# Kernel tuning notes

Hardware: AMD Instinct MI355X
Metric: run time of the kernel (lower is better)

Reference implementation:

```python
import jax, jax.numpy as jnp
import numpy as np

B, LQ, LK, SIZE, H = 8, 1024, 1024, 512, 8


def setup_inputs() -> dict:
    key = jax.random.key(0)
    ks = jax.random.split(key, 12)
    scale = 1.0 / np.sqrt(SIZE)
    x = jax.random.normal(ks[0], (B, LQ, SIZE), dtype=jnp.float32)
    states = jax.random.normal(ks[1], (B, LK, SIZE), dtype=jnp.float32)
    mask = jax.random.randint(ks[2], (B, LQ, LK), 0, 2, dtype=jnp.int32)
    # Per-head full-size projections, stacked over heads: [H, size, size]
    Wq = jax.random.normal(ks[3], (H, SIZE, SIZE), dtype=jnp.float32) * scale
    bq = jnp.zeros((H, SIZE), dtype=jnp.float32)
    Wk = jax.random.normal(ks[4], (H, SIZE, SIZE), dtype=jnp.float32) * scale
    bk = jnp.zeros((H, SIZE), dtype=jnp.float32)
    Wv = jax.random.normal(ks[5], (H, SIZE, SIZE), dtype=jnp.float32) * scale
    bv = jnp.zeros((H, SIZE), dtype=jnp.float32)
    # Output projection: Linear(size*H, size); torch weight shape [size, size*H]
    Wp = jax.random.normal(ks[6], (SIZE, SIZE * H), dtype=jnp.float32) * (1.0 / np.sqrt(SIZE * H))
    bp = jnp.zeros((SIZE,), dtype=jnp.float32)
    return {"x": x, "states": states, "mask": mask,
            "Wq": Wq, "bq": bq, "Wk": Wk, "bk": bk, "Wv": Wv, "bv": bv,
            "Wp": Wp, "bp": bp}


def reference(x, states, mask, Wq, bq, Wk, bk, Wv, bv, Wp, bp):
    # torch Linear: y = x @ W.T + b ; W is [out,in] so contract over last axis 'e'
    q = jnp.einsum('bqe,hde->bhqd', x, Wq) + bq[:, None, :]       # [B,H,Lq,D]
    k = jnp.einsum('bke,hde->bhkd', states, Wk) + bk[:, None, :]  # [B,H,Lk,D]
    v = jnp.einsum('bke,hde->bhkd', states, Wv) + bv[:, None, :]  # [B,H,Lk,D]
    scores = jnp.einsum('bhqd,bhkd->bhqk', q, k) / jnp.sqrt(jnp.float32(SIZE))
    scores = jnp.where(mask[:, None, :, :] == 0, jnp.float32(-jnp.inf), scores)
    attn = jax.nn.softmax(scores, axis=-1)                        # softmax over Lk
    ctx = jnp.einsum('bhqk,bhkd->bhqd', attn, v)                  # [B,H,Lq,D]
    # concat heads in order -> [B, Lq, H*D]
    ctx = ctx.transpose(0, 2, 1, 3).reshape(B, LQ, H * SIZE)
    return ctx @ Wp.T + bp
```

## Files before the change

kernel.cpp:

```cpp
#include <hip/hip_runtime.h>
#include <hip/hip_bf16.h>

typedef __bf16 bf16_t;
typedef __bf16 bf16x8 __attribute__((ext_vector_type(8)));
typedef float f32x4 __attribute__((ext_vector_type(4)));

#define B_DIM 8
#define LQ 1024
#define LK 1024
#define DD 512
#define NH 8
#define LB 2
#define NCH 4

static __device__ __forceinline__ f32x4 mfma_bf16(bf16x8 a, bf16x8 b, f32x4 c) {
  return __builtin_amdgcn_mfma_f32_16x16x32_bf16(a, b, c, 0, 0, 0);
}

static __device__ __forceinline__ void gld_lds16(const bf16_t* g, bf16_t* l) {
  __builtin_amdgcn_global_load_lds(
      (const __attribute__((address_space(1))) void*)g,
      (__attribute__((address_space(3))) void*)l, 16, 0, 0);
}

__global__ void cvt_pair(const float* __restrict__ s0, bf16_t* __restrict__ d0,
                         const float* __restrict__ s1, bf16_t* __restrict__ d1, int n) {
  const float* s = blockIdx.y ? s1 : s0;
  bf16_t* d = blockIdx.y ? d1 : d0;
  int i = (blockIdx.x * 256 + threadIdx.x) * 4;
  if (i < n) {
    const float4 f = *(const float4*)(s + i);
    bf16_t* p = d + i;
    p[0] = (bf16_t)f.x; p[1] = (bf16_t)f.y; p[2] = (bf16_t)f.z; p[3] = (bf16_t)f.w;
  }
}

__global__ void cvt_w3(const float* __restrict__ s0, const float* __restrict__ s1,
                       const float* __restrict__ s2, bf16_t* __restrict__ d0,
                       bf16_t* __restrict__ d1, bf16_t* __restrict__ d2, int n) {
  const float* s = (blockIdx.y == 0) ? s0 : (blockIdx.y == 1) ? s1 : s2;
  bf16_t* d = (blockIdx.y == 0) ? d0 : (blockIdx.y == 1) ? d1 : d2;
  int i = (blockIdx.x * 256 + threadIdx.x) * 4;
  if (i < n) {
    const float4 f = *(const float4*)(s + i);
    bf16_t* p = d + i;
    p[0] = (bf16_t)f.x; p[1] = (bf16_t)f.y; p[2] = (bf16_t)f.z; p[3] = (bf16_t)f.w;
  }
}

__global__ void cvt_f32_bf16(const float* __restrict__ s, bf16_t* __restrict__ d, int n) {
  int i = (blockIdx.x * 256 + threadIdx.x) * 4;
  if (i < n) {
    const float4 f = *(const float4*)(s + i);
    bf16_t* p = d + i;
    p[0] = (bf16_t)f.x; p[1] = (bf16_t)f.y; p[2] = (bf16_t)f.z; p[3] = (bf16_t)f.w;
  }
}

static __device__ __forceinline__ void gemm_core(
    const bf16_t* __restrict__ A, const bf16_t* __restrict__ B, int ld, int klen,
    int m0, int n0, bf16_t* As, bf16_t* Bs, f32x4 (&acc)[4][4])
{
  const int tid = threadIdx.x;
  const int wave = tid >> 6, lane = tid & 63;
  const int l15 = lane & 15, quad = lane >> 4;
  const int wm = (wave & 1) * 64, wn = (wave >> 1) * 64;

  const int r0 = tid >> 3;
  const int c8s = tid & 7;
  bf16_t* Asl = As + tid * 8;
  bf16_t* Bsl = Bs + tid * 8;

  for (int k0 = 0; k0 < klen; k0 += 64) {
    __syncthreads();
#pragma unroll
    for (int p = 0; p < 4; ++p) {
      const int r = r0 + p * 32;
      const int gc = ((c8s ^ (r & 7)) * 8) + k0;
      gld_lds16(A + (size_t)(m0 + r) * ld + gc, Asl + p * 2048);
      gld_lds16(B + (size_t)(n0 + r) * ld + gc, Bsl + p * 2048);
    }
    __syncthreads();
#pragma unroll
    for (int ks = 0; ks < 2; ++ks) {
      bf16x8 af[4], bfr[4];
#pragma unroll
      for (int i = 0; i < 4; ++i) {
        const int r = wm + i * 16 + l15;
        af[i] = *(const bf16x8*)&As[(r * 8 + ((ks * 4 + quad) ^ (r & 7))) * 8];
      }
#pragma unroll
      for (int j = 0; j < 4; ++j) {
        const int r = wn + j * 16 + l15;
        bfr[j] = *(const bf16x8*)&Bs[(r * 8 + ((ks * 4 + quad) ^ (r & 7))) * 8];
      }
#pragma unroll
      for (int i = 0; i < 4; ++i)
#pragma unroll
        for (int j = 0; j < 4; ++j)
          acc[i][j] = mfma_bf16(af[i], bfr[j], acc[i][j]);
    }
  }
}

__global__ __launch_bounds__(256, 4) void gemm_qkv(
    const bf16_t* __restrict__ xcb, const bf16_t* __restrict__ scb,
    const bf16_t* __restrict__ wq, const bf16_t* __restrict__ wk,
    const bf16_t* __restrict__ wv,
    const float* __restrict__ bq, const float* __restrict__ bk,
    const float* __restrict__ bv,
    bf16_t* __restrict__ Qc, bf16_t* __restrict__ Kc, bf16_t* __restrict__ Vtc)
{
  const int role = blockIdx.y >> 4, z = blockIdx.y & 15;
  const int bb = z >> 3, hh = z & 7;
  const int tx = blockIdx.x;

  const bf16_t* A; const bf16_t* Bm; const float* bias; bf16_t* C;
  int m0, n0, ldc, bias_row;
  if (role == 0) {
    A = xcb + (size_t)bb * LQ * DD; Bm = wq + (size_t)hh * DD * DD;
    bias = bq + hh * DD; C = Qc + (size_t)z * LQ * DD;
    m0 = (tx >> 2) * 128; n0 = (tx & 3) * 128; ldc = DD; bias_row = 0;
  } else if (role == 1) {
    A = scb + (size_t)bb * LK * DD; Bm = wk + (size_t)hh * DD * DD;
    bias = bk + hh * DD; C = Kc + (size_t)z * LK * DD;
    m0 = (tx >> 2) * 128; n0 = (tx & 3) * 128; ldc = DD; bias_row = 0;
  } else {
    A = wv + (size_t)hh * DD * DD; Bm = scb + (size_t)bb * LK * DD;
    bias = bv + hh * DD; C = Vtc + (size_t)z * DD * LK;
    m0 = (tx & 3) * 128; n0 = (tx >> 2) * 128; ldc = LK; bias_row = 1;
  }

  __shared__ __align__(16) bf16_t As[128 * 64];
  __shared__ __align__(16) bf16_t Bs[128 * 64];
  f32x4 acc[4][4];
#pragma unroll
  for (int i = 0; i < 4; ++i)
#pragma unroll
    for (int j = 0; j < 4; ++j) acc[i][j] = (f32x4){0.f, 0.f, 0.f, 0.f};

  gemm_core(A, Bm, DD, DD, m0, n0, As, Bs, acc);

  const int tid = threadIdx.x, wave = tid >> 6, lane = tid & 63;
  const int l15 = lane & 15, quad = lane >> 4;
  const int wm = (wave & 1) * 64, wn = (wave >> 1) * 64;
#pragma unroll
  for (int i = 0; i < 4; ++i)
#pragma unroll
    for (int j = 0; j < 4; ++j)
#pragma unroll
      for (int r = 0; r < 4; ++r) {
        const int row = m0 + wm + i * 16 + quad * 4 + r;
        const int col = n0 + wn + j * 16 + l15;
        const float v = acc[i][j][r] + (bias_row ? bias[row] : bias[col]);
        C[(size_t)row * ldc + col] = (bf16_t)v;
      }
}

__global__ __launch_bounds__(256, 4) void gemm_qk(
    const bf16_t* __restrict__ Q, const bf16_t* __restrict__ K,
    const int* __restrict__ mask, bf16_t* __restrict__ S, float* __restrict__ rs)
{
  const int z = blockIdx.z, bb = z >> 3, nt = blockIdx.y;
  const bf16_t* Az = Q + (size_t)z * LQ * DD;
  const bf16_t* Bz = K + (size_t)z * LK * DD;
  bf16_t* Sz = S + (size_t)z * LQ * LK;
  const int* mz = mask + (size_t)bb * LQ * LK;

  const int m0 = blockIdx.x * 128, n0 = nt * 128;
  __shared__ __align__(16) bf16_t As[128 * 64];
  __shared__ __align__(16) bf16_t Bs[128 * 64];
  f32x4 acc[4][4];
#pragma unroll
  for (int i = 0; i < 4; ++i)
#pragma unroll
    for (int j = 0; j < 4; ++j) acc[i][j] = (f32x4){0.f, 0.f, 0.f, 0.f};

  gemm_core(Az, Bz, DD, DD, m0, n0, As, Bs, acc);

  const int tid = threadIdx.x, wave = tid >> 6, lane = tid & 63;
  const int l15 = lane & 15, quad = lane >> 4;
  const int wm = (wave & 1) * 64, wn = (wave >> 1) * 64;
  float* rsz = rs + (((size_t)z * 8 + nt) * 2 + (wave >> 1)) * LQ;
  const float scale = 0.04419417382415922f;

#pragma unroll
  for (int i = 0; i < 4; ++i)
#pragma unroll
    for (int r = 0; r < 4; ++r) {
      const int row = m0 + wm + i * 16 + quad * 4 + r;
      float rsum = 0.f;
#pragma unroll
      for (int j = 0; j < 4; ++j) {
        const int col = n0 + wn + j * 16 + l15;
        const int mv = mz[(size_t)row * LK + col];
        const float p = mv ? __expf(acc[i][j][r] * scale) : 0.f;
        rsum += p;
        Sz[(size_t)row * LK + col] = (bf16_t)p;
      }
      rsum += __shfl_xor(rsum, 1);
      rsum += __shfl_xor(rsum, 2);
      rsum += __shfl_xor(rsum, 4);
      rsum += __shfl_xor(rsum, 8);
      if (l15 == 0) rsz[row] = rsum;
    }
}

__global__ __launch_bounds__(256, 4) void gemm_pv(
    const bf16_t* __restrict__ S, const bf16_t* __restrict__ Vt,
    const float* __restrict__ rs, bf16_t* __restrict__ ctx)
{
  const int z = blockIdx.z, bb = z >> 3, hh = z & 7;
  const bf16_t* Az = S + (size_t)z * LQ * LK;
  const bf16_t* Bz = Vt + (size_t)z * DD * LK;
  bf16_t* Cz = ctx + (size_t)bb * LQ * (NH * DD) + (size_t)hh * DD;

  const int m0 = blockIdx.x * 128, n0 = blockIdx.y * 128;
  __shared__ __align__(16) bf16_t As[128 * 64];
  __shared__ __align__(16) bf16_t Bs[128 * 64];
  __shared__ float invs[128];

  const int tid = threadIdx.x;
  if (tid < 128) {
    const float* p = rs + (size_t)z * 16 * LQ + (m0 + tid);
    float tot = 0.f;
#pragma unroll
    for (int s = 0; s < 16; ++s) tot += p[s * LQ];
    invs[tid] = 1.f / tot;
  }

  f32x4 acc[4][4];
#pragma unroll
  for (int i = 0; i < 4; ++i)
#pragma unroll
    for (int j = 0; j < 4; ++j) acc[i][j] = (f32x4){0.f, 0.f, 0.f, 0.f};

  gemm_core(Az, Bz, LK, LK, m0, n0, As, Bs, acc);

  const int wave = tid >> 6, lane = tid & 63;
  const int l15 = lane & 15, quad = lane >> 4;
  const int wm = (wave & 1) * 64, wn = (wave >> 1) * 64;

#pragma unroll
  for (int i = 0; i < 4; ++i)
#pragma unroll
    for (int r = 0; r < 4; ++r) {
      const int lrow = wm + i * 16 + quad * 4 + r;
      const float iv = invs[lrow];
#pragma unroll
      for (int j = 0; j < 4; ++j) {
        const int col = n0 + wn + j * 16 + l15;
        Cz[(size_t)(m0 + lrow) * (NH * DD) + col] = (bf16_t)(acc[i][j][r] * iv);
      }
    }
}

__global__ __launch_bounds__(256, 4) void gemm_outk(
    const bf16_t* __restrict__ ctx, const bf16_t* __restrict__ wp,
    float* __restrict__ partial)
{
  const int ks = blockIdx.z;
  const bf16_t* A = ctx + ks * 1024;
  const bf16_t* B = wp + ks * 1024;
  float* P = partial + (size_t)ks * B_DIM * LQ * DD;

  const int m0 = blockIdx.x * 128, n0 = blockIdx.y * 128;
  __shared__ __align__(16) bf16_t As[128 * 64];
  __shared__ __align__(16) bf16_t Bs[128 * 64];
  f32x4 acc[4][4];
#pragma unroll
  for (int i = 0; i < 4; ++i)
#pragma unroll
    for (int j = 0; j < 4; ++j) acc[i][j] = (f32x4){0.f, 0.f, 0.f, 0.f};

  gemm_core(A, B, NH * DD, 1024, m0, n0, As, Bs, acc);

  const int tid = threadIdx.x, wave = tid >> 6, lane = tid & 63;
  const int l15 = lane & 15, quad = lane >> 4;
  const int wm = (wave & 1) * 64, wn = (wave >> 1) * 64;
#pragma unroll
  for (int i = 0; i < 4; ++i)
#pragma unroll
    for (int j = 0; j < 4; ++j)
#pragma unroll
      for (int r = 0; r < 4; ++r) {
        const int row = m0 + wm + i * 16 + quad * 4 + r;
        const int col = n0 + wn + j * 16 + l15;
        P[(size_t)row * DD + col] = acc[i][j][r];
      }
}

__global__ void reduce_out(const float* __restrict__ p, const float* __restrict__ bp,
                           float* __restrict__ out) {
  const int N = B_DIM * LQ * DD;
  int i = (blockIdx.x * 256 + threadIdx.x) * 4;
  float4 a = *(const float4*)(p + i);
  float4 b = *(const float4*)(p + N + i);
  float4 c = *(const float4*)(p + 2 * N + i);
  float4 d = *(const float4*)(p + 3 * N + i);
  const float4 bb4 = *(const float4*)(bp + (i & 511));
  float4 r;
  r.x = a.x + b.x + c.x + d.x + bb4.x;
  r.y = a.y + b.y + c.y + d.y + bb4.y;
  r.z = a.z + b.z + c.z + d.z + bb4.z;
  r.w = a.w + b.w + c.w + d.w + bb4.w;
  *(float4*)(out + i) = r;
}

extern "C" void kernel_launch(void* const* d_in, const int* in_sizes, int n_in,
                              void* d_out, int out_size, void* d_ws, size_t ws_size,
                              hipStream_t stream) {
  const float* x      = (const float*)d_in[0];
  const float* states = (const float*)d_in[1];
  const int*   mask   = (const int*)d_in[2];
  const float* Wq     = (const float*)d_in[3];
  const float* bq     = (const float*)d_in[4];
  const float* Wk     = (const float*)d_in[5];
  const float* bk     = (const float*)d_in[6];
  const float* Wv     = (const float*)d_in[7];
  const float* bv     = (const float*)d_in[8];
  const float* Wp     = (const float*)d_in[9];
  const float* bp     = (const float*)d_in[10];
  float* out = (float*)d_out;

  char* ws = (char*)d_ws;
  bf16_t* ctxb = (bf16_t*)(ws + 0);
  bf16_t* wqb  = (bf16_t*)(ws + 67108864);
  bf16_t* wkb  = (bf16_t*)(ws + 71303168);
  bf16_t* wvb  = (bf16_t*)(ws + 75497472);
  bf16_t* Qc   = (bf16_t*)(ws + 79691776);
  bf16_t* Kc   = (bf16_t*)(ws + 96468992);
  bf16_t* Vtc  = (bf16_t*)(ws + 113246208);
  bf16_t* Sb   = (bf16_t*)(ws + 130023424);
  bf16_t* xcb  = (bf16_t*)(ws + 163577856);
  bf16_t* scb  = (bf16_t*)(ws + 165675008);
  bf16_t* wpb  = Qc;
  float*  pbuf = (float*)(ws + 96468992);
  float*  rsum = out;

  const int n_w = NH * DD * DD;
  const int n_xc = LB * LQ * DD;

  cvt_w3<<<dim3(n_w / 1024, 3), 256, 0, stream>>>(Wq, Wk, Wv, wqb, wkb, wvb, n_w);

  for (int c = 0; c < NCH; ++c) {
    const float* xc = x + (size_t)c * LB * LQ * DD;
    const float* sc = states + (size_t)c * LB * LK * DD;
    const int* mc = mask + (size_t)c * LB * LQ * LK;
    bf16_t* ctxc = ctxb + (size_t)c * LB * LQ * (NH * DD);

    cvt_pair<<<dim3(n_xc / 1024, 2), 256, 0, stream>>>(xc, xcb, sc, scb, n_xc);

    gemm_qkv<<<dim3(32, 3 * LB * NH), 256, 0, stream>>>(
        xcb, scb, wqb, wkb, wvb, bq, bk, bv, Qc, Kc, Vtc);

    gemm_qk<<<dim3(8, 8, LB * NH), 256, 0, stream>>>(Qc, Kc, mc, Sb, rsum);
    gemm_pv<<<dim3(8, 4, LB * NH), 256, 0, stream>>>(Sb, Vtc, rsum, ctxc);
  }

  cvt_f32_bf16<<<n_w / 1024, 256, 0, stream>>>(Wp, wpb, n_w);
  gemm_outk<<<dim3(64, 4, 4), 256, 0, stream>>>(ctxb, wpb, pbuf);
  reduce_out<<<(B_DIM * LQ * DD) / 1024, 256, 0, stream>>>(pbuf, bp, out);
}
```

Measured before the change: 602.3 us.

## Merge all fp32-to-bf16 conversions into one launch and swap grid axes for tile locality

All input and weight conversions (Wq, Wk, Wv, Wp, x, states) now run in one kernel launch before the chunk loop, replacing the per-chunk x/states conversions and the separate Wp conversion. The bf16 copies of Wp and x are placed in unused regions of the output buffer. Every GEMM's grid is remapped so the N tile index is blockIdx.x, which puts blocks sharing an A row-panel next to each other and may improve L2 reuse. This removes several small launches, at the cost of depending on the output buffer's scratch space not being overwritten before it is read (rsum also lives at the start of out).

```diff
diff --git a/kernel.cpp b/kernel.cpp
--- a/kernel.cpp
+++ b/kernel.cpp
@@ -23,32 +23,23 @@
       (__attribute__((address_space(3))) void*)l, 16, 0, 0);
 }
 
-__global__ void cvt_pair(const float* __restrict__ s0, bf16_t* __restrict__ d0,
-                         const float* __restrict__ s1, bf16_t* __restrict__ d1, int n) {
-  const float* s = blockIdx.y ? s1 : s0;
-  bf16_t* d = blockIdx.y ? d1 : d0;
-  int i = (blockIdx.x * 256 + threadIdx.x) * 4;
-  if (i < n) {
-    const float4 f = *(const float4*)(s + i);
-    bf16_t* p = d + i;
-    p[0] = (bf16_t)f.x; p[1] = (bf16_t)f.y; p[2] = (bf16_t)f.z; p[3] = (bf16_t)f.w;
-  }
-}
-
-__global__ void cvt_w3(const float* __restrict__ s0, const float* __restrict__ s1,
-                       const float* __restrict__ s2, bf16_t* __restrict__ d0,
-                       bf16_t* __restrict__ d1, bf16_t* __restrict__ d2, int n) {
-  const float* s = (blockIdx.y == 0) ? s0 : (blockIdx.y == 1) ? s1 : s2;
-  bf16_t* d = (blockIdx.y == 0) ? d0 : (blockIdx.y == 1) ? d1 : d2;
-  int i = (blockIdx.x * 256 + threadIdx.x) * 4;
-  if (i < n) {
-    const float4 f = *(const float4*)(s + i);
-    bf16_t* p = d + i;
-    p[0] = (bf16_t)f.x; p[1] = (bf16_t)f.y; p[2] = (bf16_t)f.z; p[3] = (bf16_t)f.w;
-  }
-}
-
-__global__ void cvt_f32_bf16(const float* __restrict__ s, bf16_t* __restrict__ d, int n) {
+__global__ void cvt_all(const float* __restrict__ s0, const float* __restrict__ s1,
+                        const float* __restrict__ s2, const float* __restrict__ s3,
+                        const float* __restrict__ s4, const float* __restrict__ s5,
+                        bf16_t* __restrict__ d0, bf16_t* __restrict__ d1,
+                        bf16_t* __restrict__ d2, bf16_t* __restrict__ d3,
+                        bf16_t* __restrict__ d4, bf16_t* __restrict__ d5,
+                        int n_w, int n_x) {
+  const int slot = blockIdx.y;
+  const float* s; bf16_t* d; int n;
+  switch (slot) {
+    case 0: s = s0; d = d0; n = n_w; break;
+    case 1: s = s1; d = d1; n = n_w; break;
+    case 2: s = s2; d = d2; n = n_w; break;
+    case 3: s = s3; d = d3; n = n_w; break;
+    case 4: s = s4; d = d4; n = n_x; break;
+    default: s = s5; d = d5; n = n_x; break;
+  }
   int i = (blockIdx.x * 256 + threadIdx.x) * 4;
   if (i < n) {
     const float4 f = *(const float4*)(s + i);
@@ -113,22 +104,21 @@
 {
   const int role = blockIdx.y >> 4, z = blockIdx.y & 15;
   const int bb = z >> 3, hh = z & 7;
-  const int tx = blockIdx.x;
 
   const bf16_t* A; const bf16_t* Bm; const float* bias; bf16_t* C;
   int m0, n0, ldc, bias_row;
   if (role == 0) {
     A = xcb + (size_t)bb * LQ * DD; Bm = wq + (size_t)hh * DD * DD;
     bias = bq + hh * DD; C = Qc + (size_t)z * LQ * DD;
-    m0 = (tx >> 2) * 128; n0 = (tx & 3) * 128; ldc = DD; bias_row = 0;
+    m0 = blockIdx.z * 128; n0 = blockIdx.x * 128; ldc = DD; bias_row = 0;
   } else if (role == 1) {
     A = scb + (size_t)bb * LK * DD; Bm = wk + (size_t)hh * DD * DD;
     bias = bk + hh * DD; C = Kc + (size_t)z * LK * DD;
-    m0 = (tx >> 2) * 128; n0 = (tx & 3) * 128; ldc = DD; bias_row = 0;
+    m0 = blockIdx.z * 128; n0 = blockIdx.x * 128; ldc = DD; bias_row = 0;
   } else {
     A = wv + (size_t)hh * DD * DD; Bm = scb + (size_t)bb * LK * DD;
     bias = bv + hh * DD; C = Vtc + (size_t)z * DD * LK;
-    m0 = (tx & 3) * 128; n0 = (tx >> 2) * 128; ldc = LK; bias_row = 1;
+    m0 = blockIdx.x * 128; n0 = blockIdx.z * 128; ldc = LK; bias_row = 1;
   }
 
   __shared__ __align__(16) bf16_t As[128 * 64];
@@ -161,13 +151,13 @@
     const bf16_t* __restrict__ Q, const bf16_t* __restrict__ K,
     const int* __restrict__ mask, bf16_t* __restrict__ S, float* __restrict__ rs)
 {
-  const int z = blockIdx.z, bb = z >> 3, nt = blockIdx.y;
+  const int z = blockIdx.z, bb = z >> 3, nt = blockIdx.x;
   const bf16_t* Az = Q + (size_t)z * LQ * DD;
   const bf16_t* Bz = K + (size_t)z * LK * DD;
   bf16_t* Sz = S + (size_t)z * LQ * LK;
   const int* mz = mask + (size_t)bb * LQ * LK;
 
-  const int m0 = blockIdx.x * 128, n0 = nt * 128;
+  const int m0 = blockIdx.y * 128, n0 = nt * 128;
   __shared__ __align__(16) bf16_t As[128 * 64];
   __shared__ __align__(16) bf16_t Bs[128 * 64];
   f32x4 acc[4][4];
@@ -215,7 +205,7 @@
   const bf16_t* Bz = Vt + (size_t)z * DD * LK;
   bf16_t* Cz = ctx + (size_t)bb * LQ * (NH * DD) + (size_t)hh * DD;
 
-  const int m0 = blockIdx.x * 128, n0 = blockIdx.y * 128;
+  const int m0 = blockIdx.y * 128, n0 = blockIdx.x * 128;
   __shared__ __align__(16) bf16_t As[128 * 64];
   __shared__ __align__(16) bf16_t Bs[128 * 64];
   __shared__ float invs[128];
@@ -264,7 +254,7 @@
   const bf16_t* B = wp + ks * 1024;
   float* P = partial + (size_t)ks * B_DIM * LQ * DD;
 
-  const int m0 = blockIdx.x * 128, n0 = blockIdx.y * 128;
+  const int m0 = blockIdx.y * 128, n0 = blockIdx.x * 128;
   __shared__ __align__(16) bf16_t As[128 * 64];
   __shared__ __align__(16) bf16_t Bs[128 * 64];
   f32x4 acc[4][4];
@@ -332,33 +322,31 @@
   bf16_t* Kc   = (bf16_t*)(ws + 96468992);
   bf16_t* Vtc  = (bf16_t*)(ws + 113246208);
   bf16_t* Sb   = (bf16_t*)(ws + 130023424);
-  bf16_t* xcb  = (bf16_t*)(ws + 163577856);
-  bf16_t* scb  = (bf16_t*)(ws + 165675008);
-  bf16_t* wpb  = Qc;
+  bf16_t* sbf  = (bf16_t*)(ws + 163577856);
   float*  pbuf = (float*)(ws + 96468992);
   float*  rsum = out;
+  bf16_t* wpb  = (bf16_t*)((char*)d_out + 1048576);
+  bf16_t* xbf  = (bf16_t*)((char*)d_out + 5242880);
 
   const int n_w = NH * DD * DD;
-  const int n_xc = LB * LQ * DD;
-
-  cvt_w3<<<dim3(n_w / 1024, 3), 256, 0, stream>>>(Wq, Wk, Wv, wqb, wkb, wvb, n_w);
+  const int n_x = B_DIM * LQ * DD;
+
+  cvt_all<<<dim3(n_x / 1024, 6), 256, 0, stream>>>(
+      Wq, Wk, Wv, Wp, x, states, wqb, wkb, wvb, wpb, xbf, sbf, n_w, n_x);
 
   for (int c = 0; c < NCH; ++c) {
-    const float* xc = x + (size_t)c * LB * LQ * DD;
-    const float* sc = states + (size_t)c * LB * LK * DD;
+    const bf16_t* xc = xbf + (size_t)c * LB * LQ * DD;
+    const bf16_t* sc = sbf + (size_t)c * LB * LK * DD;
     const int* mc = mask + (size_t)c * LB * LQ * LK;
     bf16_t* ctxc = ctxb + (size_t)c * LB * LQ * (NH * DD);
 
-    cvt_pair<<<dim3(n_xc / 1024, 2), 256, 0, stream>>>(xc, xcb, sc, scb, n_xc);
-
-    gemm_qkv<<<dim3(32, 3 * LB * NH), 256, 0, stream>>>(
-        xcb, scb, wqb, wkb, wvb, bq, bk, bv, Qc, Kc, Vtc);
+    gemm_qkv<<<dim3(4, 48, 8), 256, 0, stream>>>(
+        xc, sc, wqb, wkb, wvb, bq, bk, bv, Qc, Kc, Vtc);
 
     gemm_qk<<<dim3(8, 8, LB * NH), 256, 0, stream>>>(Qc, Kc, mc, Sb, rsum);
-    gemm_pv<<<dim3(8, 4, LB * NH), 256, 0, stream>>>(Sb, Vtc, rsum, ctxc);
-  }
-
-  cvt_f32_bf16<<<n_w / 1024, 256, 0, stream>>>(Wp, wpb, n_w);
-  gemm_outk<<<dim3(64, 4, 4), 256, 0, stream>>>(ctxb, wpb, pbuf);
+    gemm_pv<<<dim3(4, 8, LB * NH), 256, 0, stream>>>(Sb, Vtc, rsum, ctxc);
+  }
+
+  gemm_outk<<<dim3(4, 64, 4), 256, 0, stream>>>(ctxb, wpb, pbuf);
   reduce_out<<<(B_DIM * LQ * DD) / 1024, 256, 0, stream>>>(pbuf, bp, out);
 }
```

New measurement: 622.5 us. 3.4% more time.
